# Kernel tuning notes

Hardware: AMD Instinct MI355X
Metric: run time of the kernel (lower is better)

## Reference

```python
import jax, jax.numpy as jnp
import numpy as np

N_EMBED = 2048
NUM_EXPERTS = 64
TOP_K = 8
B, S = 4, 8192


def setup_inputs() -> dict:
    key = jax.random.key(0)
    ks = jax.random.split(key, 8)
    scale = 1.0 / np.sqrt(N_EMBED)
    return {
        "x": jax.random.normal(ks[0], (B, S, N_EMBED), dtype=jnp.float32),
        "eps": jax.random.normal(ks[1], (B, S, NUM_EXPERTS), dtype=jnp.float32),
        "w_router": jax.random.uniform(ks[2], (N_EMBED, NUM_EXPERTS), jnp.float32, -scale, scale),
        "b_router": jax.random.uniform(ks[3], (NUM_EXPERTS,), jnp.float32, -scale, scale),
        "w_noise": jax.random.uniform(ks[4], (N_EMBED, NUM_EXPERTS), jnp.float32, -scale, scale),
        "b_noise": jax.random.uniform(ks[5], (NUM_EXPERTS,), jnp.float32, -scale, scale),
        "w_skip": jax.random.uniform(ks[6], (N_EMBED, 1), jnp.float32, -scale, scale),
        "b_skip": jax.random.uniform(ks[7], (1,), jnp.float32, -scale, scale),
    }


def reference(x, eps, w_router, b_router, w_noise, b_noise, w_skip, b_skip):
    # Router and noise logits: [B, S, E]
    logits = jnp.einsum("bsd,de->bse", x, w_router) + b_router
    noise_logits = jnp.einsum("bsd,de->bse", x, w_noise) + b_noise
    # noisy_logits = logits + randn * softplus(noise_logits); randn passed as eps
    noisy_logits = logits + eps * jax.nn.softplus(noise_logits)
    # top-k + scatter(-inf) + softmax == softmax over top-k values scattered back
    top_vals, indices = jax.lax.top_k(noisy_logits, TOP_K)  # [B,S,K]
    gates = jax.nn.softmax(top_vals, axis=-1)  # [B,S,K]
    onehot = jax.nn.one_hot(indices, NUM_EXPERTS, dtype=x.dtype)  # [B,S,K,E]
    router_output = jnp.einsum("bsk,bske->bse", gates, onehot)  # zeros off top-k
    # Sigmoid skip gate: [B, S, 1]
    skip_prob = jax.nn.sigmoid(jnp.einsum("bsd,do->bso", x, w_skip) + b_skip)
    return router_output, indices, skip_prob
```

## Files before the change

kernel.cpp:

```cpp
#include <hip/hip_runtime.h>
#include <math.h>

#define NTOK   32768
#define D      2048
#define E      64
#define TOPK   8

#define BLOCK  256
#define TM     64
#define BK     32
#define NCHUNK (D / BK)
#define NBLK   (NTOK / TM)

#define WBF_BYTES (NCHUNK * 16384)

#define BUF_STRIDE 24576
#define WSK_OFF 49152
#define SP_OFF  57344
#define SMEM_BYTES 57600
#define LG_STR 133

#define TIE_EPS 2e-4f

typedef __bf16 bf16x8 __attribute__((ext_vector_type(8)));
typedef float  f32x4  __attribute__((ext_vector_type(4)));

#define AS1 __attribute__((address_space(1)))
#define AS3 __attribute__((address_space(3)))

__device__ __forceinline__ unsigned short f2bf_rne(float f) {
    unsigned int u = __float_as_uint(f);
    u += 0x7FFFu + ((u >> 16) & 1u);
    return (unsigned short)(u >> 16);
}

__device__ __forceinline__ void split_pack8(const float* xv, uint4& hv, uint4& lv) {
    unsigned int h[8], l[8];
#pragma unroll
    for (int j = 0; j < 8; ++j) {
        unsigned short hb = f2bf_rne(xv[j]);
        float hf = __uint_as_float(((unsigned int)hb) << 16);
        unsigned short lb = f2bf_rne(xv[j] - hf);
        h[j] = hb; l[j] = lb;
    }
    hv.x = h[0] | (h[1] << 16); hv.y = h[2] | (h[3] << 16);
    hv.z = h[4] | (h[5] << 16); hv.w = h[6] | (h[7] << 16);
    lv.x = l[0] | (l[1] << 16); lv.y = l[2] | (l[3] << 16);
    lv.z = l[4] | (l[5] << 16); lv.w = l[6] | (l[7] << 16);
}

__global__ __launch_bounds__(256) void convert_w_kernel(
    const float* __restrict__ wr, const float* __restrict__ wn, char* __restrict__ wbf)
{
    int u = blockIdx.x * 256 + threadIdx.x;
    int col  = u & 127;
    int koct = (u >> 7) & 3;
    int c    = u >> 9;
    const float* src = (col < 64)
        ? (wr + (size_t)(c * BK + koct * 8) * E + col)
        : (wn + (size_t)(c * BK + koct * 8) * E + (col - 64));
    float xv[8];
#pragma unroll
    for (int j = 0; j < 8; ++j) xv[j] = src[(size_t)j * E];
    uint4 hv, lv;
    split_pack8(xv, hv, lv);
    char* dst = wbf + (size_t)c * 16384 + (size_t)(koct * 128 + col) * 16;
    *(uint4*)dst = hv;
    *(uint4*)(dst + 8192) = lv;
}

__global__ __launch_bounds__(BLOCK, 2) void router_kernel(
    const float* __restrict__ x, const float* __restrict__ eps,
    const char* __restrict__ wbf,
    const float* __restrict__ b_router, const float* __restrict__ b_noise,
    const float* __restrict__ w_skip, const float* __restrict__ b_skip,
    float* __restrict__ out_router, float* __restrict__ out_idx,
    float* __restrict__ out_skip, int* __restrict__ flags, int cap)
{
    __shared__ __attribute__((aligned(16))) char smem[SMEM_BYTES];
    const int tid = threadIdx.x;
    const int tokBase = blockIdx.x * TM;

    const int lane = tid & 63;
    const int wv   = __builtin_amdgcn_readfirstlane(tid >> 6);
    const int q    = lane >> 4;
    const int m    = lane & 15;

    const int tokA  = tid >> 2;
    const int koctA = tid & 3;
    const int fragA = (koctA << 6) + (tokA ^ (koctA << 2));
    const float* xptr = x + (size_t)(tokBase + tokA) * D + koctA * 8;

    f32x4 acc[4][2];
#pragma unroll
    for (int tt = 0; tt < 4; ++tt)
#pragma unroll
        for (int cw = 0; cw < 2; ++cw) acc[tt][cw] = (f32x4){0.f, 0.f, 0.f, 0.f};
    float skipAcc = 0.f;

    float* wsk = (float*)(smem + WSK_OFF);

    auto issueB = [&](int c, int buf) {
        const char* src = wbf + (size_t)c * 16384;
        char* dstbase = smem + buf * BUF_STRIDE + 8192;
#pragma unroll
        for (int r = 0; r < 4; ++r) {
            int seg = r * 4 + wv;
            __builtin_amdgcn_global_load_lds(
                (const AS1 unsigned int*)(src + seg * 1024 + lane * 16),
                (AS3 unsigned int*)(dstbase + seg * 1024), 16, 0, 0);
        }
    };

    auto storeA = [&](int buf, float4 a0, float4 a1) {
        float xv[8] = {a0.x, a0.y, a0.z, a0.w, a1.x, a1.y, a1.z, a1.w};
        uint4 hv, lv;
        split_pack8(xv, hv, lv);
        char* ab = smem + buf * BUF_STRIDE;
        *(uint4*)(ab + fragA * 16) = hv;
        *(uint4*)(ab + 4096 + fragA * 16) = lv;
    };

    auto skipFma = [&](float4 a0, float4 a1, int c) {
        const float* wk = wsk + c * BK + koctA * 8;
        skipAcc = fmaf(a0.x, wk[0], skipAcc); skipAcc = fmaf(a0.y, wk[1], skipAcc);
        skipAcc = fmaf(a0.z, wk[2], skipAcc); skipAcc = fmaf(a0.w, wk[3], skipAcc);
        skipAcc = fmaf(a1.x, wk[4], skipAcc); skipAcc = fmaf(a1.y, wk[5], skipAcc);
        skipAcc = fmaf(a1.z, wk[6], skipAcc); skipAcc = fmaf(a1.w, wk[7], skipAcc);
    };

    auto compute = [&](int buf) {
        const char* ab = smem + buf * BUF_STRIDE;
        const char* bb = ab + 8192;
        uint4 ah[4], al[4], bh[2], bl[2];
#pragma unroll
        for (int tt = 0; tt < 4; ++tt) {
            int f = (q << 6) + (((tt << 4) + m) ^ (q << 2));
            ah[tt] = *(const uint4*)(ab + f * 16);
            al[tt] = *(const uint4*)(ab + 4096 + f * 16);
        }
#pragma unroll
        for (int cw = 0; cw < 2; ++cw) {
            int f = (q << 7) + (wv << 5) + (cw << 4) + m;
            bh[cw] = *(const uint4*)(bb + f * 16);
            bl[cw] = *(const uint4*)(bb + 8192 + f * 16);
        }
#pragma unroll
        for (int tt = 0; tt < 4; ++tt)
#pragma unroll
            for (int cw = 0; cw < 2; ++cw) {
                bf16x8 Ah = __builtin_bit_cast(bf16x8, ah[tt]);
                bf16x8 Al = __builtin_bit_cast(bf16x8, al[tt]);
                bf16x8 Bh = __builtin_bit_cast(bf16x8, bh[cw]);
                bf16x8 Bl = __builtin_bit_cast(bf16x8, bl[cw]);
                acc[tt][cw] = __builtin_amdgcn_mfma_f32_16x16x32_bf16(Ah, Bh, acc[tt][cw], 0, 0, 0);
                acc[tt][cw] = __builtin_amdgcn_mfma_f32_16x16x32_bf16(Ah, Bl, acc[tt][cw], 0, 0, 0);
                acc[tt][cw] = __builtin_amdgcn_mfma_f32_16x16x32_bf16(Al, Bh, acc[tt][cw], 0, 0, 0);
            }
    };

#pragma unroll
    for (int r = 0; r < 2; ++r) {
        int i4 = tid + 256 * r;
        ((float4*)wsk)[i4] = ((const float4*)w_skip)[i4];
    }
    float4 ra0 = *(const float4*)(xptr);
    float4 ra1 = *(const float4*)(xptr + 4);
    issueB(0, 0);
    storeA(0, ra0, ra1);
    __syncthreads();
    skipFma(ra0, ra1, 0);

    for (int c = 0; c < NCHUNK; ++c) {
        int cur = c & 1;
        float4 rb0, rb1;
        if (c + 1 < NCHUNK) {
            rb0 = *(const float4*)(xptr + (c + 1) * BK);
            rb1 = *(const float4*)(xptr + (c + 1) * BK + 4);
            issueB(c + 1, cur ^ 1);
        }
        compute(cur);
        if (c + 1 < NCHUNK) {
            storeA(cur ^ 1, rb0, rb1);
            skipFma(rb0, rb1, c + 1);
        }
        __syncthreads();
    }

    float* lg = (float*)smem;
#pragma unroll
    for (int tt = 0; tt < 4; ++tt)
#pragma unroll
        for (int cw = 0; cw < 2; ++cw) {
#pragma unroll
            for (int reg = 0; reg < 4; ++reg) {
                int token = tt * 16 + q * 4 + reg;
                int col = wv * 32 + cw * 16 + m;
                lg[token * LG_STR + col] = acc[tt][cw][reg];
            }
        }

    skipAcc += __shfl_xor(skipAcc, 1);
    skipAcc += __shfl_xor(skipAcc, 2);
    if ((tid & 3) == 0) ((float*)(smem + SP_OFF))[tokA] = skipAcc;
    __syncthreads();

    if (tid < 64) {
        const int t = tid;
        const int tok = tokBase + t;
        float* row = lg + t * LG_STR;

        float sv = ((float*)(smem + SP_OFF))[t] + b_skip[0];
        out_skip[tok] = 1.f / (1.f + expf(-sv));

        const float4* epsr = (const float4*)(eps + (size_t)tok * E);
#pragma unroll 4
        for (int e4 = 0; e4 < 16; ++e4) {
            float4 ep = epsr[e4];
            float epv[4] = {ep.x, ep.y, ep.z, ep.w};
#pragma unroll
            for (int u2 = 0; u2 < 4; ++u2) {
                int e = e4 * 4 + u2;
                float lgv = row[e] + b_router[e];
                float nl  = row[64 + e] + b_noise[e];
                float sp  = fmaxf(nl, 0.f) + log1pf(expf(-fabsf(nl)));
                row[e] = lgv + epv[u2] * sp;
            }
        }

        float vals[9];
        int idxs[8];
        for (int p = 0; p < 9; ++p) {
            float best = -INFINITY;
            int bi = 0;
            for (int e = 0; e < 64; ++e) {
                float v = row[e];
                if (v > best) { best = v; bi = e; }
            }
            vals[p] = best;
            if (p < 8) idxs[p] = bi;
            row[bi] = -INFINITY;
        }

        float mg = 1e30f;
#pragma unroll
        for (int p = 0; p < 8; ++p) mg = fminf(mg, vals[p] - vals[p + 1]);
        if (mg < TIE_EPS) {
            int slot = atomicAdd(flags, 1);
            if (slot < cap) flags[2 + slot] = tok;
        }

        float mx = vals[0];
        float g[8], s = 0.f;
#pragma unroll
        for (int p = 0; p < 8; ++p) { g[p] = expf(vals[p] - mx); s += g[p]; }
        float inv = 1.f / s;

        float* rrow = row + 64;
#pragma unroll
        for (int e = 0; e < 64; ++e) rrow[e] = 0.f;
#pragma unroll
        for (int p = 0; p < 8; ++p) rrow[idxs[p]] = g[p] * inv;
#pragma unroll
        for (int e4 = 0; e4 < 16; ++e4) {
            float4 o = make_float4(rrow[e4 * 4], rrow[e4 * 4 + 1],
                                   rrow[e4 * 4 + 2], rrow[e4 * 4 + 3]);
            *(float4*)(out_router + (size_t)tok * E + e4 * 4) = o;
        }
        float4 i0 = make_float4((float)idxs[0], (float)idxs[1], (float)idxs[2], (float)idxs[3]);
        float4 i1 = make_float4((float)idxs[4], (float)idxs[5], (float)idxs[6], (float)idxs[7]);
        *(float4*)(out_idx + (size_t)tok * TOPK)     = i0;
        *(float4*)(out_idx + (size_t)tok * TOPK + 4) = i1;
    }
}

__global__ __launch_bounds__(256) void fixup_kernel(
    const float* __restrict__ x, const float* __restrict__ eps,
    const float* __restrict__ w_router, const float* __restrict__ b_router,
    const float* __restrict__ w_noise, const float* __restrict__ b_noise,
    float* __restrict__ out_router, float* __restrict__ out_idx,
    const int* __restrict__ flags, int cap)
{
    __shared__ double smR[4][64];
    __shared__ double smN[4][64];
    __shared__ double noisy[64];
    const int tid  = threadIdx.x;
    const int lane = tid & 63;
    const int qw   = tid >> 6;

    int count = flags[0];
    if (count > cap) count = cap;

    for (int i = blockIdx.x; i < count; i += gridDim.x) {
        int tok = flags[2 + i];
        const float4* xr4 = (const float4*)(x + (size_t)tok * D + qw * 512);
        const float* wrB = w_router + (size_t)(qw * 512) * E + lane;
        const float* wnB = w_noise  + (size_t)(qw * 512) * E + lane;

        double pr0 = 0, pr1 = 0, pr2 = 0, pr3 = 0;
        double pn0 = 0, pn1 = 0, pn2 = 0, pn3 = 0;
        for (int it = 0; it < 128; ++it) {
            float4 xv = xr4[it];
            const float* wr = wrB + (size_t)(it * 4) * E;
            const float* wn = wnB + (size_t)(it * 4) * E;
            pr0 += (double)xv.x * (double)wr[0];
            pr1 += (double)xv.y * (double)wr[E];
            pr2 += (double)xv.z * (double)wr[2 * E];
            pr3 += (double)xv.w * (double)wr[3 * E];
            pn0 += (double)xv.x * (double)wn[0];
            pn1 += (double)xv.y * (double)wn[E];
            pn2 += (double)xv.z * (double)wn[2 * E];
            pn3 += (double)xv.w * (double)wn[3 * E];
        }
        smR[qw][lane] = (pr0 + pr1) + (pr2 + pr3);
        smN[qw][lane] = (pn0 + pn1) + (pn2 + pn3);
        __syncthreads();

        if (tid < 64) {
            double lgv = smR[0][tid] + smR[1][tid] + smR[2][tid] + smR[3][tid] + (double)b_router[tid];
            double nl  = smN[0][tid] + smN[1][tid] + smN[2][tid] + smN[3][tid] + (double)b_noise[tid];
            double sp  = fmax(nl, 0.0) + log1p(exp(-fabs(nl)));
            noisy[tid] = lgv + (double)eps[(size_t)tok * E + tid] * sp;
        }
        __syncthreads();

        if (tid == 0) {
            double tmp[64];
            for (int j = 0; j < 64; ++j) tmp[j] = noisy[j];
            double vals[8]; int idxs[8];
            for (int p = 0; p < 8; ++p) {
                double best = -1e300; int bi = 0;
                for (int j = 0; j < 64; ++j)
                    if (tmp[j] > best) { best = tmp[j]; bi = j; }
                vals[p] = best; idxs[p] = bi; tmp[bi] = -1e300;
            }
            double mx = vals[0], s = 0.0, g[8];
            for (int p = 0; p < 8; ++p) { g[p] = exp(vals[p] - mx); s += g[p]; }
            float rowv[64];
            for (int j = 0; j < 64; ++j) rowv[j] = 0.f;
            for (int p = 0; p < 8; ++p) rowv[idxs[p]] = (float)(g[p] / s);
            for (int j = 0; j < 64; ++j) out_router[(size_t)tok * E + j] = rowv[j];
            for (int p = 0; p < 8; ++p) out_idx[(size_t)tok * TOPK + p] = (float)idxs[p];
        }
        __syncthreads();
    }
}

extern "C" void kernel_launch(void* const* d_in, const int* in_sizes, int n_in,
                              void* d_out, int out_size, void* d_ws, size_t ws_size,
                              hipStream_t stream) {
    const float* x        = (const float*)d_in[0];
    const float* eps      = (const float*)d_in[1];
    const float* w_router = (const float*)d_in[2];
    const float* b_router = (const float*)d_in[3];
    const float* w_noise  = (const float*)d_in[4];
    const float* b_noise  = (const float*)d_in[5];
    const float* w_skip   = (const float*)d_in[6];
    const float* b_skip   = (const float*)d_in[7];

    float* out = (float*)d_out;
    float* out_router = out;
    float* out_idx    = out + (size_t)NTOK * E;
    float* out_skip   = out_idx + (size_t)NTOK * TOPK;

    char* wbf  = (char*)d_ws;
    int* flags = (int*)((char*)d_ws + WBF_BYTES);
    int cap = 0;
    if (ws_size > WBF_BYTES + 16) {
        size_t c = (ws_size - WBF_BYTES - 8) / 4;
        cap = (c > 16384) ? 16384 : (int)c;
    }

    hipMemsetAsync((char*)d_ws + WBF_BYTES, 0, 8, stream);

    convert_w_kernel<<<dim3(128), dim3(256), 0, stream>>>(w_router, w_noise, wbf);

    router_kernel<<<dim3(NBLK), dim3(BLOCK), 0, stream>>>(
        x, eps, wbf, b_router, b_noise, w_skip, b_skip,
        out_router, out_idx, out_skip, flags, cap);

    fixup_kernel<<<dim3(512), dim3(256), 0, stream>>>(
        x, eps, w_router, b_router, w_noise, b_noise,
        out_router, out_idx, flags, cap);
}
```

Measured before the change: 543.6 us.

## Load router weight fragments directly into registers and prefetch x two chunks ahead

Each wave now reads its B (router/noise weight) fragments straight from global memory into registers instead of staging them through LDS with global_load_lds, so only the A tile stays in shared memory. The x loads are software-pipelined two chunks ahead through a register queue. Shared memory shrinks from about 57 KB to about 42 KB. The tie-break epsilon is halved and the fp64 fallback loop is unrolled by 2. The aim is to cut LDS traffic and footprint, at the cost of more VGPRs and repeated global or L2 reads of the weights by every block.

```diff
diff --git a/kernel.cpp b/kernel.cpp
--- a/kernel.cpp
+++ b/kernel.cpp
@@ -14,19 +14,18 @@
 
 #define WBF_BYTES (NCHUNK * 16384)
 
-#define BUF_STRIDE 24576
-#define WSK_OFF 49152
-#define SP_OFF  57344
-#define SMEM_BYTES 57600
-#define LG_STR 133
-
-#define TIE_EPS 2e-4f
+#define ABUF0   0
+#define ABUF1   8192
+#define LG_OFF  0
+#define LG_STR  133
+#define WSK_OFF 34048
+#define SP_OFF  42240
+#define SMEM_BYTES 42496
+
+#define TIE_EPS 1e-4f
 
 typedef __bf16 bf16x8 __attribute__((ext_vector_type(8)));
 typedef float  f32x4  __attribute__((ext_vector_type(4)));
-
-#define AS1 __attribute__((address_space(1)))
-#define AS3 __attribute__((address_space(3)))
 
 __device__ __forceinline__ unsigned short f2bf_rne(float f) {
     unsigned int u = __float_as_uint(f);
@@ -82,7 +81,7 @@
     const int tokBase = blockIdx.x * TM;
 
     const int lane = tid & 63;
-    const int wv   = __builtin_amdgcn_readfirstlane(tid >> 6);
+    const int wv   = tid >> 6;
     const int q    = lane >> 4;
     const int m    = lane & 15;
 
@@ -100,15 +99,13 @@
 
     float* wsk = (float*)(smem + WSK_OFF);
 
-    auto issueB = [&](int c, int buf) {
+    auto loadB = [&](int c, uint4* bh, uint4* bl) {
         const char* src = wbf + (size_t)c * 16384;
-        char* dstbase = smem + buf * BUF_STRIDE + 8192;
-#pragma unroll
-        for (int r = 0; r < 4; ++r) {
-            int seg = r * 4 + wv;
-            __builtin_amdgcn_global_load_lds(
-                (const AS1 unsigned int*)(src + seg * 1024 + lane * 16),
-                (AS3 unsigned int*)(dstbase + seg * 1024), 16, 0, 0);
+#pragma unroll
+        for (int cw = 0; cw < 2; ++cw) {
+            int f = (q << 7) + (wv << 5) + (cw << 4) + m;
+            bh[cw] = *(const uint4*)(src + f * 16);
+            bl[cw] = *(const uint4*)(src + 8192 + f * 16);
         }
     };
 
@@ -116,7 +113,7 @@
         float xv[8] = {a0.x, a0.y, a0.z, a0.w, a1.x, a1.y, a1.z, a1.w};
         uint4 hv, lv;
         split_pack8(xv, hv, lv);
-        char* ab = smem + buf * BUF_STRIDE;
+        char* ab = smem + (buf ? ABUF1 : ABUF0);
         *(uint4*)(ab + fragA * 16) = hv;
         *(uint4*)(ab + 4096 + fragA * 16) = lv;
     };
@@ -129,21 +126,14 @@
         skipAcc = fmaf(a1.z, wk[6], skipAcc); skipAcc = fmaf(a1.w, wk[7], skipAcc);
     };
 
-    auto compute = [&](int buf) {
-        const char* ab = smem + buf * BUF_STRIDE;
-        const char* bb = ab + 8192;
-        uint4 ah[4], al[4], bh[2], bl[2];
+    auto compute = [&](int buf, const uint4* bh, const uint4* bl) {
+        const char* ab = smem + (buf ? ABUF1 : ABUF0);
+        uint4 ah[4], al[4];
 #pragma unroll
         for (int tt = 0; tt < 4; ++tt) {
             int f = (q << 6) + (((tt << 4) + m) ^ (q << 2));
             ah[tt] = *(const uint4*)(ab + f * 16);
             al[tt] = *(const uint4*)(ab + 4096 + f * 16);
-        }
-#pragma unroll
-        for (int cw = 0; cw < 2; ++cw) {
-            int f = (q << 7) + (wv << 5) + (cw << 4) + m;
-            bh[cw] = *(const uint4*)(bb + f * 16);
-            bl[cw] = *(const uint4*)(bb + 8192 + f * 16);
         }
 #pragma unroll
         for (int tt = 0; tt < 4; ++tt)
@@ -164,30 +154,36 @@
         int i4 = tid + 256 * r;
         ((float4*)wsk)[i4] = ((const float4*)w_skip)[i4];
     }
-    float4 ra0 = *(const float4*)(xptr);
-    float4 ra1 = *(const float4*)(xptr + 4);
-    issueB(0, 0);
-    storeA(0, ra0, ra1);
+    float4 xq[2][2];
+    xq[0][0] = *(const float4*)(xptr);
+    xq[0][1] = *(const float4*)(xptr + 4);
+    xq[1][0] = *(const float4*)(xptr + BK);
+    xq[1][1] = *(const float4*)(xptr + BK + 4);
+    uint4 bh[2], bl[2], bhn[2], bln[2];
+    loadB(0, bh, bl);
+    storeA(0, xq[0][0], xq[0][1]);
+    skipFma(xq[0][0], xq[0][1], 0);
     __syncthreads();
-    skipFma(ra0, ra1, 0);
 
     for (int c = 0; c < NCHUNK; ++c) {
-        int cur = c & 1;
-        float4 rb0, rb1;
+        if (c + 1 < NCHUNK) loadB(c + 1, bhn, bln);
+        float4 xn0, xn1;
+        if (c + 2 < NCHUNK) {
+            xn0 = *(const float4*)(xptr + (c + 2) * BK);
+            xn1 = *(const float4*)(xptr + (c + 2) * BK + 4);
+        }
+        compute(c & 1, bh, bl);
         if (c + 1 < NCHUNK) {
-            rb0 = *(const float4*)(xptr + (c + 1) * BK);
-            rb1 = *(const float4*)(xptr + (c + 1) * BK + 4);
-            issueB(c + 1, cur ^ 1);
-        }
-        compute(cur);
-        if (c + 1 < NCHUNK) {
-            storeA(cur ^ 1, rb0, rb1);
-            skipFma(rb0, rb1, c + 1);
-        }
+            storeA((c + 1) & 1, xq[(c + 1) & 1][0], xq[(c + 1) & 1][1]);
+            skipFma(xq[(c + 1) & 1][0], xq[(c + 1) & 1][1], c + 1);
+        }
+        if (c + 2 < NCHUNK) { xq[c & 1][0] = xn0; xq[c & 1][1] = xn1; }
+#pragma unroll
+        for (int cw = 0; cw < 2; ++cw) { bh[cw] = bhn[cw]; bl[cw] = bln[cw]; }
         __syncthreads();
     }
 
-    float* lg = (float*)smem;
+    float* lg = (float*)(smem + LG_OFF);
 #pragma unroll
     for (int tt = 0; tt < 4; ++tt)
 #pragma unroll
@@ -299,6 +295,7 @@
 
         double pr0 = 0, pr1 = 0, pr2 = 0, pr3 = 0;
         double pn0 = 0, pn1 = 0, pn2 = 0, pn3 = 0;
+#pragma unroll 2
         for (int it = 0; it < 128; ++it) {
             float4 xv = xr4[it];
             const float* wr = wrB + (size_t)(it * 4) * E;
```

Measured after the change: 544.9 us. About the same (+0.2%).
